# Kernel optimization log

Measured on AMD Instinct MI355X. Metric: run time of the kernel, lower is better.

## Reference

```python
import jax, jax.numpy as jnp
import numpy as np

B, N, H, HS, PH = 8, 384, 12, 768, 64
D = HS // H  # 64


def _ln(x, g, b, eps=1e-5):
    m = jnp.mean(x, axis=-1, keepdims=True)
    v = jnp.mean(jnp.square(x - m), axis=-1, keepdims=True)
    return (x - m) * jax.lax.rsqrt(v + eps) * g + b


def setup_inputs() -> dict:
    key = jax.random.key(0)
    ks = jax.random.split(key, 16)
    s = 0.02
    return {
        "nodes": jax.random.normal(ks[0], (B, N, HS), jnp.float32),
        "bias": jnp.zeros((B, 1, 1, N), jnp.float32),
        "paths": jax.random.normal(ks[1], (B, N, N, PH), jnp.float32),
        "Wq": jax.random.normal(ks[2], (HS, HS), jnp.float32) * s,
        "bq": jnp.zeros((HS,), jnp.float32),
        "Wk": jax.random.normal(ks[3], (HS, HS), jnp.float32) * s,
        "bk": jnp.zeros((HS,), jnp.float32),
        "Wv": jax.random.normal(ks[4], (HS, HS), jnp.float32) * s,
        "bv": jnp.zeros((HS,), jnp.float32),
        "Wsk": jax.random.normal(ks[5], (PH, D), jnp.float32) * s,
        "bsk": jnp.zeros((D,), jnp.float32),
        "Wsv": jax.random.normal(ks[6], (PH, D), jnp.float32) * s,
        "bsv": jnp.zeros((D,), jnp.float32),
        "Wo": jax.random.normal(ks[7], (HS, HS), jnp.float32) * s,
        "bo": jnp.zeros((HS,), jnp.float32),
        "ln_g": jnp.ones((HS,), jnp.float32),
        "ln_b": jnp.zeros((HS,), jnp.float32),
        "pln_g": jnp.ones((PH,), jnp.float32),
        "pln_b": jnp.zeros((PH,), jnp.float32),
    }


def reference(nodes, bias, paths, Wq, bq, Wk, bk, Wv, bv, Wsk, bsk, Wsv, bsv,
              Wo, bo, ln_g, ln_b, pln_g, pln_b):
    # q/k/v projections, split heads -> (B, H, N, D)
    def split(x):
        return x.reshape(B, N, H, D).transpose(0, 2, 1, 3)

    q = split(nodes @ Wq + bq)
    k = split(nodes @ Wk + bk)
    v = split(nodes @ Wv + bv)

    p = _ln(paths, pln_g, pln_b)            # (B, N, N, PH)
    struct_k = p @ Wsk + bsk                # (B, N, N, D)
    struct_v = p @ Wsv + bsv                # (B, N, N, D)

    q = q * (D ** -0.5)
    w = jnp.einsum('bhid,bhjd->bhij', q, k)           # content scores
    w = w + jnp.einsum('bhid,bijd->bhij', q, struct_k)  # structural scores
    w = jax.nn.softmax(w + bias, axis=-1)             # (B, H, N, N)

    out = jnp.einsum('bhij,bhjd->bhid', w, v) \
        + jnp.einsum('bhij,bijd->bhid', w, struct_v)  # (B, H, N, D)
    out = out.transpose(0, 2, 1, 3).reshape(B, N, HS)
    out = jax.nn.relu(out @ Wo + bo)
    # dropout p=0.0 -> identity
    return _ln(nodes + out, ln_g, ln_b), w
```

## Files before the change

kernel.cpp:

```cpp
#include <hip/hip_runtime.h>
#include <hip/hip_bf16.h>

typedef __hip_bfloat16 bf16;
typedef __attribute__((ext_vector_type(8))) short short8b;
typedef __attribute__((ext_vector_type(4))) float f32x4;

#define BB  8
#define NN  384
#define HH  12
#define HSZ 768
#define DD  64
#define PHH 64
#define PSTR 386
#define SWS  194

__device__ __forceinline__ float bflo(unsigned u){ union{unsigned q; float f;} c; c.q = u << 16;        return c.f; }
__device__ __forceinline__ float bfhi(unsigned u){ union{unsigned q; float f;} c; c.q = u & 0xffff0000u; return c.f; }

__device__ __forceinline__ unsigned pk2bf(float lo, float hi){
    union{float f; unsigned u;} a, b; a.f = lo; b.f = hi;
    unsigned ua = a.u + 0x7fffu + ((a.u >> 16) & 1u);
    unsigned ub = b.u + 0x7fffu + ((b.u >> 16) & 1u);
    return (ua >> 16) | (ub & 0xffff0000u);
}

union U8 { uint4 u; short8b v; };

__device__ __forceinline__ void pk32(const float4* p, uint4* o){
    #pragma unroll
    for (int e = 0; e < 4; e++) {
        float4 x = p[2*e], y = p[2*e+1];
        o[e].x = pk2bf(x.x, x.y); o[e].y = pk2bf(x.z, x.w);
        o[e].z = pk2bf(y.x, y.y); o[e].w = pk2bf(y.z, y.w);
    }
}

__global__ __launch_bounds__(256) void k_qkv(
    const float* __restrict__ nodes,
    const float* __restrict__ Wq, const float* __restrict__ bq,
    const float* __restrict__ Wk, const float* __restrict__ bk,
    const float* __restrict__ Wv, const float* __restrict__ bv,
    float* __restrict__ oq, float* __restrict__ okk, float* __restrict__ ov)
{
    const int which = blockIdx.z;
    const float* __restrict__ W   = which==0 ? Wq : (which==1 ? Wk : Wv);
    const float* __restrict__ bia = which==0 ? bq : (which==1 ? bk : bv);
    float* __restrict__ out       = which==0 ? oq : (which==1 ? okk : ov);
    const float scale = which==0 ? 0.125f : 1.0f;

    __shared__ __align__(16) unsigned Alds[128*20];
    __shared__ __align__(16) unsigned Blds[128*20];

    const int row0 = blockIdx.x * 128;
    const int col0 = blockIdx.y * 128;
    const int tid  = threadIdx.x;
    const int wv   = tid >> 6, lane = tid & 63;
    const int wm   = wv & 1,  wn   = wv >> 1;
    const int fr   = lane & 15, kg = lane >> 4;

    f32x4 acc[4][4];
    #pragma unroll
    for (int i=0;i<4;i++){
        #pragma unroll
        for (int j=0;j<4;j++){ acc[i][j][0]=0.f; acc[i][j][1]=0.f; acc[i][j][2]=0.f; acc[i][j][3]=0.f; }
    }

    for (int k0 = 0; k0 < HSZ; k0 += 32) {
        {
            const int m = tid >> 1, kh = tid & 1;
            const float4* ap = reinterpret_cast<const float4*>(nodes + (size_t)(row0 + m)*HSZ + k0 + kh*16);
            float4 a0 = ap[0], a1 = ap[1], a2 = ap[2], a3 = ap[3];
            uint4 p0, p1;
            p0.x = pk2bf(a0.x,a0.y); p0.y = pk2bf(a0.z,a0.w);
            p0.z = pk2bf(a1.x,a1.y); p0.w = pk2bf(a1.z,a1.w);
            p1.x = pk2bf(a2.x,a2.y); p1.y = pk2bf(a2.z,a2.w);
            p1.z = pk2bf(a3.x,a3.y); p1.w = pk2bf(a3.z,a3.w);
            *reinterpret_cast<uint4*>(&Alds[m*20 + kh*8    ]) = p0;
            *reinterpret_cast<uint4*>(&Alds[m*20 + kh*8 + 4]) = p1;
        }
        {
            const int n = tid & 127, kq = tid >> 7;
            const float* wp = W + (size_t)(k0 + kq*16)*HSZ + col0 + n;
            float x[16];
            #pragma unroll
            for (int j = 0; j < 16; j++) x[j] = wp[(size_t)j*HSZ];
            uint4 p0, p1;
            p0.x = pk2bf(x[0],x[1]);   p0.y = pk2bf(x[2],x[3]);
            p0.z = pk2bf(x[4],x[5]);   p0.w = pk2bf(x[6],x[7]);
            p1.x = pk2bf(x[8],x[9]);   p1.y = pk2bf(x[10],x[11]);
            p1.z = pk2bf(x[12],x[13]); p1.w = pk2bf(x[14],x[15]);
            *reinterpret_cast<uint4*>(&Blds[n*20 + kq*8    ]) = p0;
            *reinterpret_cast<uint4*>(&Blds[n*20 + kq*8 + 4]) = p1;
        }
        __syncthreads();
        U8 au[4], bu[4];
        #pragma unroll
        for (int t = 0; t < 4; t++) {
            au[t].u = *reinterpret_cast<const uint4*>(&Alds[(wm*64 + t*16 + fr)*20 + kg*4]);
            bu[t].u = *reinterpret_cast<const uint4*>(&Blds[(wn*64 + t*16 + fr)*20 + kg*4]);
        }
        #pragma unroll
        for (int mt = 0; mt < 4; mt++)
            #pragma unroll
            for (int nt = 0; nt < 4; nt++)
                acc[mt][nt] = __builtin_amdgcn_mfma_f32_16x16x32_bf16(
                    au[mt].v, bu[nt].v, acc[mt][nt], 0, 0, 0);
        __syncthreads();
    }
    #pragma unroll
    for (int nt = 0; nt < 4; nt++) {
        const int col = col0 + wn*64 + nt*16 + fr;
        const int h = col >> 6, d = col & 63;
        const float bv_ = bia[col];
        #pragma unroll
        for (int mt = 0; mt < 4; mt++) {
            #pragma unroll
            for (int r = 0; r < 4; r++) {
                const int m = row0 + wm*64 + mt*16 + kg*4 + r;
                const int b_ = m / NN, n_ = m % NN;
                out[(((size_t)b_*HH + h)*NN + n_)*DD + d] = (acc[mt][nt][r] + bv_) * scale;
            }
        }
    }
}

__global__ __launch_bounds__(256) void k_qsk(
    const float* __restrict__ q_s, const float* __restrict__ Wsk,
    float* __restrict__ qsk)
{
    __shared__ __align__(16) unsigned Alds[128*36];
    __shared__ __align__(16) unsigned Blds[64*36];
    const int row0 = blockIdx.x * 128;
    const int tid = threadIdx.x;
    const int wv = tid >> 6, lane = tid & 63;
    const int fr = lane & 15, kg = lane >> 4;

    {
        const int m = tid >> 1, kh = tid & 1;
        const float4* ap = reinterpret_cast<const float4*>(q_s + (size_t)(row0 + m)*DD + kh*32);
        uint4 pa[4]; pk32(ap, pa);
        #pragma unroll
        for (int e = 0; e < 4; e++)
            *reinterpret_cast<uint4*>(&Alds[m*36 + kh*16 + 4*e]) = pa[e];
    }
    {
        const int n = tid & 63, kq = tid >> 6;
        const float4* bp = reinterpret_cast<const float4*>(Wsk + (size_t)n*DD + kq*16);
        float4 b0 = bp[0], b1 = bp[1], b2 = bp[2], b3 = bp[3];
        uint4 p0, p1;
        p0.x = pk2bf(b0.x,b0.y); p0.y = pk2bf(b0.z,b0.w);
        p0.z = pk2bf(b1.x,b1.y); p0.w = pk2bf(b1.z,b1.w);
        p1.x = pk2bf(b2.x,b2.y); p1.y = pk2bf(b2.z,b2.w);
        p1.z = pk2bf(b3.x,b3.y); p1.w = pk2bf(b3.z,b3.w);
        *reinterpret_cast<uint4*>(&Blds[n*36 + kq*8    ]) = p0;
        *reinterpret_cast<uint4*>(&Blds[n*36 + kq*8 + 4]) = p1;
    }
    __syncthreads();

    f32x4 acc[2][4];
    #pragma unroll
    for (int i=0;i<2;i++){
        #pragma unroll
        for (int j=0;j<4;j++){ acc[i][j][0]=0.f; acc[i][j][1]=0.f; acc[i][j][2]=0.f; acc[i][j][3]=0.f; }
    }
    #pragma unroll
    for (int ks = 0; ks < 2; ks++) {
        U8 au[2], bu[4];
        #pragma unroll
        for (int mt = 0; mt < 2; mt++)
            au[mt].u = *reinterpret_cast<const uint4*>(&Alds[(wv*32 + mt*16 + fr)*36 + ks*16 + kg*4]);
        #pragma unroll
        for (int nt = 0; nt < 4; nt++)
            bu[nt].u = *reinterpret_cast<const uint4*>(&Blds[(nt*16 + fr)*36 + ks*16 + kg*4]);
        #pragma unroll
        for (int mt = 0; mt < 2; mt++)
            #pragma unroll
            for (int nt = 0; nt < 4; nt++)
                acc[mt][nt] = __builtin_amdgcn_mfma_f32_16x16x32_bf16(
                    au[mt].v, bu[nt].v, acc[mt][nt], 0, 0, 0);
    }
    #pragma unroll
    for (int nt = 0; nt < 4; nt++) {
        #pragma unroll
        for (int mt = 0; mt < 2; mt++) {
            #pragma unroll
            for (int r = 0; r < 4; r++) {
                const int m = row0 + wv*32 + mt*16 + kg*4 + r;
                qsk[(size_t)m*DD + nt*16 + fr] = acc[mt][nt][r];
            }
        }
    }
}

__global__ __launch_bounds__(256) void k_scores(
    const float* __restrict__ q_s, const float* __restrict__ kk_, float* __restrict__ wc)
{
    const int bh = blockIdx.z;
    __shared__ __align__(16) unsigned Alds[128*36];
    __shared__ __align__(16) unsigned Blds[128*36];
    const int i0 = blockIdx.x * 128, j0 = blockIdx.y * 128;
    const int tid = threadIdx.x;
    const int wv  = tid >> 6, lane = tid & 63;
    const int wm  = wv & 1,  wn   = wv >> 1;
    const int fr  = lane & 15, kg = lane >> 4;

    {
        const int m = tid >> 1, kh = tid & 1;
        const float4* ap = reinterpret_cast<const float4*>(q_s + ((size_t)bh*NN + i0 + m)*DD + kh*32);
        const float4* bp = reinterpret_cast<const float4*>(kk_ + ((size_t)bh*NN + j0 + m)*DD + kh*32);
        uint4 pa[4], pbq[4];
        pk32(ap, pa);
        pk32(bp, pbq);
        #pragma unroll
        for (int e = 0; e < 4; e++) {
            *reinterpret_cast<uint4*>(&Alds[m*36 + kh*16 + 4*e]) = pa[e];
            *reinterpret_cast<uint4*>(&Blds[m*36 + kh*16 + 4*e]) = pbq[e];
        }
    }
    __syncthreads();

    f32x4 acc[4][4];
    #pragma unroll
    for (int i=0;i<4;i++){
        #pragma unroll
        for (int j=0;j<4;j++){ acc[i][j][0]=0.f; acc[i][j][1]=0.f; acc[i][j][2]=0.f; acc[i][j][3]=0.f; }
    }
    #pragma unroll
    for (int ks = 0; ks < 2; ks++) {
        U8 au[4], bu[4];
        #pragma unroll
        for (int t = 0; t < 4; t++) {
            au[t].u = *reinterpret_cast<const uint4*>(&Alds[(wm*64 + t*16 + fr)*36 + ks*16 + kg*4]);
            bu[t].u = *reinterpret_cast<const uint4*>(&Blds[(wn*64 + t*16 + fr)*36 + ks*16 + kg*4]);
        }
        #pragma unroll
        for (int mt = 0; mt < 4; mt++)
            #pragma unroll
            for (int nt = 0; nt < 4; nt++)
                acc[mt][nt] = __builtin_amdgcn_mfma_f32_16x16x32_bf16(
                    au[mt].v, bu[nt].v, acc[mt][nt], 0, 0, 0);
    }
    #pragma unroll
    for (int nt = 0; nt < 4; nt++) {
        const int j = j0 + wn*64 + nt*16 + fr;
        #pragma unroll
        for (int mt = 0; mt < 4; mt++) {
            #pragma unroll
            for (int r = 0; r < 4; r++) {
                const int i = i0 + wm*64 + mt*16 + kg*4 + r;
                wc[((size_t)bh*NN + i)*NN + j] = acc[mt][nt][r];
            }
        }
    }
}

__global__ __launch_bounds__(384) void k_soft(
    const float* __restrict__ paths, const float* __restrict__ bias,
    const float* __restrict__ pg, const float* __restrict__ pb,
    const float* __restrict__ wc, const float* __restrict__ qsk,
    float* __restrict__ pagg, float* __restrict__ w_out)
{
    const int bi = blockIdx.x;
    const int b = bi / NN, i = bi % NN;
    __shared__ __align__(16) unsigned pLNT[32 * PSTR];
    __shared__ __align__(16) unsigned sw32[16 * SWS];
    __shared__ __align__(16) unsigned qskA[16 * 36];
    __shared__ float redM[6][16];
    __shared__ float redS[6][16];
    __shared__ float pgf[64], pbf[64];
    const int tid  = threadIdx.x;
    const int wv   = tid >> 6, lane = tid & 63;
    const int g    = lane >> 4, c = lane & 15;
    const int jbase = wv*64 + c;

    float x[64];
    {
        const float4* src = reinterpret_cast<const float4*>(paths + ((size_t)bi * NN + tid) * PHH);
        #pragma unroll
        for (int t = 0; t < 16; t++) {
            float4 u = src[t];
            x[4*t]=u.x; x[4*t+1]=u.y; x[4*t+2]=u.z; x[4*t+3]=u.w;
        }
    }
    float wcv[4][4], biasj[4];
    #pragma unroll
    for (int nt = 0; nt < 4; nt++) {
        const int j = jbase + nt*16;
        biasj[nt] = bias[b*NN + j];
        #pragma unroll
        for (int r = 0; r < 4; r++) {
            const int h = g*4 + r;
            wcv[nt][r] = (h < HH) ? wc[((size_t)(b*HH + h)*NN + i)*NN + j] : 0.f;
        }
    }
    if (tid < 64) { pgf[tid] = pg[tid]; pbf[tid] = pb[tid]; }
    {
        const int h = tid >> 5, t2 = tid & 31;
        const size_t r0 = ((size_t)(b*HH + h)*NN + i)*DD;
        const float q0 = qsk[r0 + 2*t2], q1 = qsk[r0 + 2*t2 + 1];
        qskA[h*36 + t2] = pk2bf(q0, q1);
        if (tid < 144) qskA[432 + tid] = 0u;
    }
    __syncthreads();

    {
        float m0 = 0.f, m1 = 0.f;
        #pragma unroll
        for (int t = 0; t < 32; t++){ m0 += x[2*t]; m1 += x[2*t+1]; }
        const float m = (m0+m1)*(1.f/64.f);
        float v0 = 0.f, v1 = 0.f;
        #pragma unroll
        for (int t = 0; t < 32; t++){
            float a = x[2*t]-m, d = x[2*t+1]-m;
            v0 = fmaf(a,a,v0); v1 = fmaf(d,d,v1);
        }
        const float rs = rsqrtf((v0+v1)*(1.f/64.f) + 1e-5f);
        #pragma unroll
        for (int w = 0; w < 32; w++){
            const float lo = (x[2*w  ]-m)*rs*pgf[2*w  ] + pbf[2*w  ];
            const float hi = (x[2*w+1]-m)*rs*pgf[2*w+1] + pbf[2*w+1];
            pLNT[w*PSTR + tid] = pk2bf(lo, hi);
        }
    }
    __syncthreads();

    f32x4 sc[4];
    #pragma unroll
    for (int nt=0;nt<4;nt++){ sc[nt][0]=0.f; sc[nt][1]=0.f; sc[nt][2]=0.f; sc[nt][3]=0.f; }
    #pragma unroll
    for (int kh = 0; kh < 2; kh++) {
        U8 a; a.u = *reinterpret_cast<const uint4*>(&qskA[c*36 + kh*16 + g*4]);
        #pragma unroll
        for (int nt = 0; nt < 4; nt++) {
            const unsigned* pb_ = &pLNT[(kh*16 + g*4)*PSTR + jbase + nt*16];
            uint4 bw;
            bw.x = pb_[0]; bw.y = pb_[PSTR]; bw.z = pb_[2*PSTR]; bw.w = pb_[3*PSTR];
            U8 bb; bb.u = bw;
            sc[nt] = __builtin_amdgcn_mfma_f32_16x16x32_bf16(a.v, bb.v, sc[nt], 0, 0, 0);
        }
    }
    #pragma unroll
    for (int nt = 0; nt < 4; nt++)
        #pragma unroll
        for (int r = 0; r < 4; r++)
            sc[nt][r] += wcv[nt][r] + biasj[nt];

    float e_[4][4], inv_[4];
    {
        float mr[4];
        #pragma unroll
        for (int r = 0; r < 4; r++) {
            float m2 = fmaxf(fmaxf(sc[0][r], sc[1][r]), fmaxf(sc[2][r], sc[3][r]));
            #pragma unroll
            for (int o = 1; o <= 8; o <<= 1) m2 = fmaxf(m2, __shfl_xor(m2, o, 64));
            mr[r] = m2;
        }
        if (c == 0) {
            #pragma unroll
            for (int r = 0; r < 4; r++) redM[wv][g*4 + r] = mr[r];
        }
        __syncthreads();
        #pragma unroll
        for (int r = 0; r < 4; r++) {
            float Mv = redM[0][g*4 + r];
            #pragma unroll
            for (int w2 = 1; w2 < 6; w2++) Mv = fmaxf(Mv, redM[w2][g*4 + r]);
            float s2 = 0.f;
            #pragma unroll
            for (int nt = 0; nt < 4; nt++){ e_[nt][r] = __expf(sc[nt][r] - Mv); s2 += e_[nt][r]; }
            #pragma unroll
            for (int o = 1; o <= 8; o <<= 1) s2 += __shfl_xor(s2, o, 64);
            mr[r] = s2;
        }
        if (c == 0) {
            #pragma unroll
            for (int r = 0; r < 4; r++) redS[wv][g*4 + r] = mr[r];
        }
        __syncthreads();
        #pragma unroll
        for (int r = 0; r < 4; r++) {
            float Sv = redS[0][g*4 + r];
            #pragma unroll
            for (int w2 = 1; w2 < 6; w2++) Sv += redS[w2][g*4 + r];
            inv_[r] = 1.f / Sv;
        }
    }
    #pragma unroll
    for (int nt = 0; nt < 4; nt++) {
        const int j = jbase + nt*16;
        #pragma unroll
        for (int r = 0; r < 4; r++) {
            const int h = g*4 + r;
            const float wgt = e_[nt][r] * inv_[r];
            if (h < HH) w_out[((size_t)(b*HH + h)*NN + i)*NN + j] = wgt;
            const float oth = __shfl_xor(wgt, 1, 64);
            if ((c & 1) == 0) sw32[h*SWS + (j >> 1)] = pk2bf(wgt, oth);
        }
    }
    __syncthreads();

    if (wv < 4) {
        f32x4 pa; pa[0]=0.f; pa[1]=0.f; pa[2]=0.f; pa[3]=0.f;
        const int prow = 8*wv + (c >> 1);
        const bool hi = (c & 1);
        #pragma unroll 4
        for (int kt = 0; kt < 12; kt++) {
            uint2 a0 = *reinterpret_cast<const uint2*>(&sw32[c*SWS + kt*16 + g*4]);
            uint2 a1 = *reinterpret_cast<const uint2*>(&sw32[c*SWS + kt*16 + g*4 + 2]);
            U8 af; af.u.x = a0.x; af.u.y = a0.y; af.u.z = a1.x; af.u.w = a1.y;
            const unsigned* pr = &pLNT[prow*PSTR + 32*kt + 8*g];
            uint2 w01 = *reinterpret_cast<const uint2*>(&pr[0]);
            uint2 w23 = *reinterpret_cast<const uint2*>(&pr[2]);
            uint2 w45 = *reinterpret_cast<const uint2*>(&pr[4]);
            uint2 w67 = *reinterpret_cast<const uint2*>(&pr[6]);
            uint4 bw;
            if (hi) {
                bw.x = (w01.x >> 16) | (w01.y & 0xffff0000u);
                bw.y = (w23.x >> 16) | (w23.y & 0xffff0000u);
                bw.z = (w45.x >> 16) | (w45.y & 0xffff0000u);
                bw.w = (w67.x >> 16) | (w67.y & 0xffff0000u);
            } else {
                bw.x = (w01.x & 0xffffu) | (w01.y << 16);
                bw.y = (w23.x & 0xffffu) | (w23.y << 16);
                bw.z = (w45.x & 0xffffu) | (w45.y << 16);
                bw.w = (w67.x & 0xffffu) | (w67.y << 16);
            }
            U8 bf_; bf_.u = bw;
            pa = __builtin_amdgcn_mfma_f32_16x16x32_bf16(af.v, bf_.v, pa, 0, 0, 0);
        }
        #pragma unroll
        for (int r = 0; r < 4; r++) {
            const int h = g*4 + r;
            if (h < HH)
                pagg[((size_t)(b*HH + h)*NN + i)*DD + 16*wv + c] = pa[r];
        }
    }
}

__global__ __launch_bounds__(256) void k_av(
    const float* __restrict__ w, const float* __restrict__ v_,
    const float* __restrict__ pagg, const float* __restrict__ Wsv,
    const float* __restrict__ bsv, float* __restrict__ attn)
{
    const int bh = blockIdx.y;
    const int b = bh / HH, h = bh % HH;
    const int i0 = blockIdx.x * 128;
    __shared__ __align__(16) unsigned Alds[128*36];
    __shared__ __align__(16) unsigned Blds[64*36];
    const int tid = threadIdx.x;
    const int wv  = tid >> 6, lane = tid & 63;
    const int fr  = lane & 15, kg = lane >> 4;

    f32x4 acc[2][4];
    #pragma unroll
    for (int i=0;i<2;i++){
        #pragma unroll
        for (int j=0;j<4;j++){ acc[i][j][0]=0.f; acc[i][j][1]=0.f; acc[i][j][2]=0.f; acc[i][j][3]=0.f; }
    }

    for (int step = 0; step < 7; step++) {
        const int j0 = step * 64;
        {
            const int m = tid >> 1, kh = tid & 1;
            const float4* ap = (step < 6)
                ? reinterpret_cast<const float4*>(w    + ((size_t)bh*NN + i0 + m)*NN  + j0 + kh*32)
                : reinterpret_cast<const float4*>(pagg + ((size_t)bh*NN + i0 + m)*PHH + kh*32);
            uint4 pa[4];
            pk32(ap, pa);
            #pragma unroll
            for (int e = 0; e < 4; e++)
                *reinterpret_cast<uint4*>(&Alds[m*36 + kh*16 + 4*e]) = pa[e];
        }
        {
            const int d = tid & 63, kq = tid >> 6;
            const float* vp = (step < 6)
                ? (v_  + ((size_t)bh*NN + j0 + kq*16)*DD + d)
                : (Wsv + (size_t)(kq*16)*DD + d);
            float x[16];
            #pragma unroll
            for (int t = 0; t < 16; t++) x[t] = vp[(size_t)t*DD];
            uint4 p0,p1;
            p0.x=pk2bf(x[0],x[1]);   p0.y=pk2bf(x[2],x[3]);
            p0.z=pk2bf(x[4],x[5]);   p0.w=pk2bf(x[6],x[7]);
            p1.x=pk2bf(x[8],x[9]);   p1.y=pk2bf(x[10],x[11]);
            p1.z=pk2bf(x[12],x[13]); p1.w=pk2bf(x[14],x[15]);
            *reinterpret_cast<uint4*>(&Blds[d*36 + kq*8    ]) = p0;
            *reinterpret_cast<uint4*>(&Blds[d*36 + kq*8 + 4]) = p1;
        }
        __syncthreads();
        #pragma unroll
        for (int ks = 0; ks < 2; ks++) {
            U8 au[2], bu[4];
            #pragma unroll
            for (int mt = 0; mt < 2; mt++)
                au[mt].u = *reinterpret_cast<const uint4*>(&Alds[(wv*32 + mt*16 + fr)*36 + ks*16 + kg*4]);
            #pragma unroll
            for (int nt = 0; nt < 4; nt++)
                bu[nt].u = *reinterpret_cast<const uint4*>(&Blds[(nt*16 + fr)*36 + ks*16 + kg*4]);
            #pragma unroll
            for (int mt = 0; mt < 2; mt++)
                #pragma unroll
                for (int nt = 0; nt < 4; nt++)
                    acc[mt][nt] = __builtin_amdgcn_mfma_f32_16x16x32_bf16(
                        au[mt].v, bu[nt].v, acc[mt][nt], 0, 0, 0);
        }
        __syncthreads();
    }
    #pragma unroll
    for (int nt = 0; nt < 4; nt++) {
        const int d = nt*16 + fr;
        const float bv_ = bsv[d];
        #pragma unroll
        for (int mt = 0; mt < 2; mt++) {
            #pragma unroll
            for (int r = 0; r < 4; r++) {
                const int i = i0 + wv*32 + mt*16 + kg*4 + r;
                attn[((size_t)b*NN + i)*HSZ + h*DD + d] = acc[mt][nt][r] + bv_;
            }
        }
    }
}

__global__ __launch_bounds__(256) void k_proj(
    const float* __restrict__ attn, const float* __restrict__ Wo,
    const float* __restrict__ bo, const float* __restrict__ nodes,
    float* __restrict__ tres)
{
    __shared__ __align__(16) unsigned Alds[128*20];
    __shared__ __align__(16) unsigned Blds[128*20];

    const int row0 = blockIdx.x * 128;
    const int col0 = blockIdx.y * 128;
    const int tid  = threadIdx.x;
    const int wv   = tid >> 6, lane = tid & 63;
    const int wm   = wv & 1,  wn   = wv >> 1;
    const int fr   = lane & 15, kg = lane >> 4;

    f32x4 acc[4][4];
    #pragma unroll
    for (int i=0;i<4;i++){
        #pragma unroll
        for (int j=0;j<4;j++){ acc[i][j][0]=0.f; acc[i][j][1]=0.f; acc[i][j][2]=0.f; acc[i][j][3]=0.f; }
    }

    for (int k0 = 0; k0 < HSZ; k0 += 32) {
        {
            const int m = tid >> 1, kh = tid & 1;
            const float4* ap = reinterpret_cast<const float4*>(attn + (size_t)(row0 + m)*HSZ + k0 + kh*16);
            float4 a0 = ap[0], a1 = ap[1], a2 = ap[2], a3 = ap[3];
            uint4 p0, p1;
            p0.x = pk2bf(a0.x,a0.y); p0.y = pk2bf(a0.z,a0.w);
            p0.z = pk2bf(a1.x,a1.y); p0.w = pk2bf(a1.z,a1.w);
            p1.x = pk2bf(a2.x,a2.y); p1.y = pk2bf(a2.z,a2.w);
            p1.z = pk2bf(a3.x,a3.y); p1.w = pk2bf(a3.z,a3.w);
            *reinterpret_cast<uint4*>(&Alds[m*20 + kh*8    ]) = p0;
            *reinterpret_cast<uint4*>(&Alds[m*20 + kh*8 + 4]) = p1;
        }
        {
            const int n = tid & 127, kq = tid >> 7;
            const float* wp = Wo + (size_t)(k0 + kq*16)*HSZ + col0 + n;
            float x[16];
            #pragma unroll
            for (int j = 0; j < 16; j++) x[j] = wp[(size_t)j*HSZ];
            uint4 p0, p1;
            p0.x = pk2bf(x[0],x[1]);   p0.y = pk2bf(x[2],x[3]);
            p0.z = pk2bf(x[4],x[5]);   p0.w = pk2bf(x[6],x[7]);
            p1.x = pk2bf(x[8],x[9]);   p1.y = pk2bf(x[10],x[11]);
            p1.z = pk2bf(x[12],x[13]); p1.w = pk2bf(x[14],x[15]);
            *reinterpret_cast<uint4*>(&Blds[n*20 + kq*8    ]) = p0;
            *reinterpret_cast<uint4*>(&Blds[n*20 + kq*8 + 4]) = p1;
        }
        __syncthreads();
        U8 au[4], bu[4];
        #pragma unroll
        for (int t = 0; t < 4; t++) {
            au[t].u = *reinterpret_cast<const uint4*>(&Alds[(wm*64 + t*16 + fr)*20 + kg*4]);
            bu[t].u = *reinterpret_cast<const uint4*>(&Blds[(wn*64 + t*16 + fr)*20 + kg*4]);
        }
        #pragma unroll
        for (int mt = 0; mt < 4; mt++)
            #pragma unroll
            for (int nt = 0; nt < 4; nt++)
                acc[mt][nt] = __builtin_amdgcn_mfma_f32_16x16x32_bf16(
                    au[mt].v, bu[nt].v, acc[mt][nt], 0, 0, 0);
        __syncthreads();
    }
    #pragma unroll
    for (int nt = 0; nt < 4; nt++) {
        const int col = col0 + wn*64 + nt*16 + fr;
        const float bov = bo[col];
        #pragma unroll
        for (int mt = 0; mt < 4; mt++) {
            #pragma unroll
            for (int r = 0; r < 4; r++) {
                const int m = row0 + wm*64 + mt*16 + kg*4 + r;
                const float val = fmaxf(acc[mt][nt][r] + bov, 0.f) + nodes[(size_t)m*HSZ + col];
                tres[(size_t)m*HSZ + col] = val;
            }
        }
    }
}

__global__ __launch_bounds__(256) void k_ln(
    const float* __restrict__ tres, const float* __restrict__ g,
    const float* __restrict__ bta, float* __restrict__ out0)
{
    const int row  = blockIdx.x * 4 + (threadIdx.x >> 6);
    const int lane = threadIdx.x & 63;
    const float4* x4 = reinterpret_cast<const float4*>(tres + (size_t)row * HSZ);
    float4 v[3];
    #pragma unroll
    for (int t = 0; t < 3; t++) v[t] = x4[lane + t*64];
    float s = 0.f;
    #pragma unroll
    for (int t = 0; t < 3; t++) s += v[t].x + v[t].y + v[t].z + v[t].w;
    #pragma unroll
    for (int o = 32; o > 0; o >>= 1) s += __shfl_xor(s, o, 64);
    const float m = s * (1.f/768.f);
    float vs = 0.f;
    #pragma unroll
    for (int t = 0; t < 3; t++) {
        float a = v[t].x-m, b = v[t].y-m, c = v[t].z-m, d = v[t].w-m;
        vs += a*a + b*b + c*c + d*d;
    }
    #pragma unroll
    for (int o = 32; o > 0; o >>= 1) vs += __shfl_xor(vs, o, 64);
    const float rs = rsqrtf(vs * (1.f/768.f) + 1e-5f);
    const float4* g4 = reinterpret_cast<const float4*>(g);
    const float4* b4 = reinterpret_cast<const float4*>(bta);
    float4* o4 = reinterpret_cast<float4*>(out0 + (size_t)row * HSZ);
    #pragma unroll
    for (int t = 0; t < 3; t++) {
        const int idx = lane + t*64;
        float4 gg = g4[idx], bb = b4[idx], o;
        o.x = (v[t].x-m)*rs*gg.x + bb.x;
        o.y = (v[t].y-m)*rs*gg.y + bb.y;
        o.z = (v[t].z-m)*rs*gg.z + bb.z;
        o.w = (v[t].w-m)*rs*gg.w + bb.w;
        o4[idx] = o;
    }
}

extern "C" void kernel_launch(void* const* d_in, const int* in_sizes, int n_in,
                              void* d_out, int out_size, void* d_ws, size_t ws_size,
                              hipStream_t stream)
{
    (void)in_sizes; (void)n_in; (void)out_size; (void)ws_size;
    const float* nodes = (const float*)d_in[0];
    const float* bias  = (const float*)d_in[1];
    const float* paths = (const float*)d_in[2];
    const float* Wq = (const float*)d_in[3];
    const float* bq = (const float*)d_in[4];
    const float* Wk = (const float*)d_in[5];
    const float* bk = (const float*)d_in[6];
    const float* Wv = (const float*)d_in[7];
    const float* bv = (const float*)d_in[8];
    const float* Wsk= (const float*)d_in[9];
    const float* Wsv= (const float*)d_in[11];
    const float* bsv= (const float*)d_in[12];
    const float* Wo = (const float*)d_in[13];
    const float* bo = (const float*)d_in[14];
    const float* lng= (const float*)d_in[15];
    const float* lnb= (const float*)d_in[16];
    const float* plg= (const float*)d_in[17];
    const float* plb= (const float*)d_in[18];

    float* ws   = (float*)d_ws;
    float* q_s  = ws;
    float* kbuf = ws + 2359296;
    float* vbuf = ws + 4718592;
    float* qsk  = ws + 7077888;
    float* wc   = ws + 9474048;
    float* attn = q_s;
    float* pagg = kbuf;
    float* tres = wc;

    float* out0 = (float*)d_out;
    float* wout = out0 + (size_t)BB*NN*HSZ;

    hipLaunchKernelGGL(k_qkv,    dim3(24,6,3), dim3(256), 0, stream,
                       nodes, Wq,bq, Wk,bk, Wv,bv, q_s, kbuf, vbuf);
    hipLaunchKernelGGL(k_qsk,    dim3(288),    dim3(256), 0, stream,
                       q_s, Wsk, qsk);
    hipLaunchKernelGGL(k_scores, dim3(3,3,96), dim3(256), 0, stream,
                       q_s, kbuf, wc);
    hipLaunchKernelGGL(k_soft,   dim3(3072),   dim3(384), 0, stream,
                       paths, bias, plg, plb, wc, qsk, pagg, wout);
    hipLaunchKernelGGL(k_av,     dim3(3,96),   dim3(256), 0, stream,
                       wout, vbuf, pagg, Wsv, bsv, attn);
    hipLaunchKernelGGL(k_proj,   dim3(24,6),   dim3(256), 0, stream,
                       attn, Wo, bo, nodes, tres);
    hipLaunchKernelGGL(k_ln,     dim3(768),    dim3(256), 0, stream,
                       tres, lng, lnb, out0);
}
```

Baseline: 283.6 us.

## Double k_soft block size, splitting each path row LayerNorm across two threads

```diff
diff --git a/kernel.cpp b/kernel.cpp
--- a/kernel.cpp
+++ b/kernel.cpp
@@ -254,7 +254,7 @@
     }
 }
 
-__global__ __launch_bounds__(384) void k_soft(
+__global__ __launch_bounds__(768) void k_soft(
     const float* __restrict__ paths, const float* __restrict__ bias,
     const float* __restrict__ pg, const float* __restrict__ pb,
     const float* __restrict__ wc, const float* __restrict__ qsk,
@@ -265,26 +265,28 @@
     __shared__ __align__(16) unsigned pLNT[32 * PSTR];
     __shared__ __align__(16) unsigned sw32[16 * SWS];
     __shared__ __align__(16) unsigned qskA[16 * 36];
-    __shared__ float redM[6][16];
-    __shared__ float redS[6][16];
+    __shared__ float redM[12][16];
+    __shared__ float redS[12][16];
     __shared__ float pgf[64], pbf[64];
     const int tid  = threadIdx.x;
     const int wv   = tid >> 6, lane = tid & 63;
     const int g    = lane >> 4, c = lane & 15;
-    const int jbase = wv*64 + c;
-
-    float x[64];
+    const int jbase = wv*32 + c;
+
+    const int jrow = tid >> 1, hf = tid & 1;
+    float x[32];
     {
-        const float4* src = reinterpret_cast<const float4*>(paths + ((size_t)bi * NN + tid) * PHH);
-        #pragma unroll
-        for (int t = 0; t < 16; t++) {
+        const float4* src = reinterpret_cast<const float4*>(
+            paths + ((size_t)bi * NN + jrow) * PHH + hf*32);
+        #pragma unroll
+        for (int t = 0; t < 8; t++) {
             float4 u = src[t];
             x[4*t]=u.x; x[4*t+1]=u.y; x[4*t+2]=u.z; x[4*t+3]=u.w;
         }
     }
-    float wcv[4][4], biasj[4];
-    #pragma unroll
-    for (int nt = 0; nt < 4; nt++) {
+    float wcv[2][4], biasj[2];
+    #pragma unroll
+    for (int nt = 0; nt < 2; nt++) {
         const int j = jbase + nt*16;
         biasj[nt] = bias[b*NN + j];
         #pragma unroll
@@ -294,7 +296,7 @@
         }
     }
     if (tid < 64) { pgf[tid] = pg[tid]; pbf[tid] = pb[tid]; }
-    {
+    if (tid < 384) {
         const int h = tid >> 5, t2 = tid & 31;
         const size_t r0 = ((size_t)(b*HH + h)*NN + i)*DD;
         const float q0 = qsk[r0 + 2*t2], q1 = qsk[r0 + 2*t2 + 1];
@@ -304,34 +306,35 @@
     __syncthreads();
 
     {
-        float m0 = 0.f, m1 = 0.f;
-        #pragma unroll
-        for (int t = 0; t < 32; t++){ m0 += x[2*t]; m1 += x[2*t+1]; }
-        const float m = (m0+m1)*(1.f/64.f);
-        float v0 = 0.f, v1 = 0.f;
-        #pragma unroll
-        for (int t = 0; t < 32; t++){
-            float a = x[2*t]-m, d = x[2*t+1]-m;
-            v0 = fmaf(a,a,v0); v1 = fmaf(d,d,v1);
-        }
-        const float rs = rsqrtf((v0+v1)*(1.f/64.f) + 1e-5f);
-        #pragma unroll
-        for (int w = 0; w < 32; w++){
-            const float lo = (x[2*w  ]-m)*rs*pgf[2*w  ] + pbf[2*w  ];
-            const float hi = (x[2*w+1]-m)*rs*pgf[2*w+1] + pbf[2*w+1];
-            pLNT[w*PSTR + tid] = pk2bf(lo, hi);
+        float m0 = 0.f;
+        #pragma unroll
+        for (int t = 0; t < 32; t++) m0 += x[t];
+        const float mo = __shfl_xor(m0, 1, 64);
+        const float m = (m0 + mo) * (1.f/64.f);
+        float v0 = 0.f;
+        #pragma unroll
+        for (int t = 0; t < 32; t++){ float d = x[t]-m; v0 = fmaf(d,d,v0); }
+        const float vo = __shfl_xor(v0, 1, 64);
+        const float rs = rsqrtf((v0+vo)*(1.f/64.f) + 1e-5f);
+        #pragma unroll
+        for (int t = 0; t < 16; t++){
+            const int w = hf*16 + t;
+            const int ph = hf*32 + 2*t;
+            const float lo = (x[2*t  ]-m)*rs*pgf[ph  ] + pbf[ph  ];
+            const float hi = (x[2*t+1]-m)*rs*pgf[ph+1] + pbf[ph+1];
+            pLNT[w*PSTR + jrow] = pk2bf(lo, hi);
         }
     }
     __syncthreads();
 
-    f32x4 sc[4];
-    #pragma unroll
-    for (int nt=0;nt<4;nt++){ sc[nt][0]=0.f; sc[nt][1]=0.f; sc[nt][2]=0.f; sc[nt][3]=0.f; }
+    f32x4 sc[2];
+    #pragma unroll
+    for (int nt=0;nt<2;nt++){ sc[nt][0]=0.f; sc[nt][1]=0.f; sc[nt][2]=0.f; sc[nt][3]=0.f; }
     #pragma unroll
     for (int kh = 0; kh < 2; kh++) {
         U8 a; a.u = *reinterpret_cast<const uint4*>(&qskA[c*36 + kh*16 + g*4]);
         #pragma unroll
-        for (int nt = 0; nt < 4; nt++) {
+        for (int nt = 0; nt < 2; nt++) {
             const unsigned* pb_ = &pLNT[(kh*16 + g*4)*PSTR + jbase + nt*16];
             uint4 bw;
             bw.x = pb_[0]; bw.y = pb_[PSTR]; bw.z = pb_[2*PSTR]; bw.w = pb_[3*PSTR];
@@ -340,17 +343,17 @@
         }
     }
     #pragma unroll
-    for (int nt = 0; nt < 4; nt++)
+    for (int nt = 0; nt < 2; nt++)
         #pragma unroll
         for (int r = 0; r < 4; r++)
             sc[nt][r] += wcv[nt][r] + biasj[nt];
 
-    float e_[4][4], inv_[4];
+    float e_[2][4], inv_[4];
     {
         float mr[4];
         #pragma unroll
         for (int r = 0; r < 4; r++) {
-            float m2 = fmaxf(fmaxf(sc[0][r], sc[1][r]), fmaxf(sc[2][r], sc[3][r]));
+            float m2 = fmaxf(sc[0][r], sc[1][r]);
             #pragma unroll
             for (int o = 1; o <= 8; o <<= 1) m2 = fmaxf(m2, __shfl_xor(m2, o, 64));
             mr[r] = m2;
@@ -364,10 +367,10 @@
         for (int r = 0; r < 4; r++) {
             float Mv = redM[0][g*4 + r];
             #pragma unroll
-            for (int w2 = 1; w2 < 6; w2++) Mv = fmaxf(Mv, redM[w2][g*4 + r]);
+            for (int w2 = 1; w2 < 12; w2++) Mv = fmaxf(Mv, redM[w2][g*4 + r]);
             float s2 = 0.f;
             #pragma unroll
-            for (int nt = 0; nt < 4; nt++){ e_[nt][r] = __expf(sc[nt][r] - Mv); s2 += e_[nt][r]; }
+            for (int nt = 0; nt < 2; nt++){ e_[nt][r] = __expf(sc[nt][r] - Mv); s2 += e_[nt][r]; }
             #pragma unroll
             for (int o = 1; o <= 8; o <<= 1) s2 += __shfl_xor(s2, o, 64);
             mr[r] = s2;
@@ -381,12 +384,12 @@
         for (int r = 0; r < 4; r++) {
             float Sv = redS[0][g*4 + r];
             #pragma unroll
-            for (int w2 = 1; w2 < 6; w2++) Sv += redS[w2][g*4 + r];
+            for (int w2 = 1; w2 < 12; w2++) Sv += redS[w2][g*4 + r];
             inv_[r] = 1.f / Sv;
         }
     }
     #pragma unroll
-    for (int nt = 0; nt < 4; nt++) {
+    for (int nt = 0; nt < 2; nt++) {
         const int j = jbase + nt*16;
         #pragma unroll
         for (int r = 0; r < 4; r++) {
@@ -684,7 +687,7 @@
                        q_s, Wsk, qsk);
     hipLaunchKernelGGL(k_scores, dim3(3,3,96), dim3(256), 0, stream,
                        q_s, kbuf, wc);
-    hipLaunchKernelGGL(k_soft,   dim3(3072),   dim3(384), 0, stream,
+    hipLaunchKernelGGL(k_soft,   dim3(3072),   dim3(768), 0, stream,
                        paths, bias, plg, plb, wc, qsk, pagg, wout);
     hipLaunchKernelGGL(k_av,     dim3(3,96),   dim3(256), 0, stream,
                        wout, vbuf, pagg, Wsv, bsv, attn);
```

Result: no change. 280.1 us, median of 2 (-1.2%).

## Process two query rows per k_soft block, prefetching the second paths row

Applied to the files above, without the earlier changes.

```diff
diff --git a/kernel.cpp b/kernel.cpp
--- a/kernel.cpp
+++ b/kernel.cpp
@@ -260,8 +260,9 @@
     const float* __restrict__ wc, const float* __restrict__ qsk,
     float* __restrict__ pagg, float* __restrict__ w_out)
 {
-    const int bi = blockIdx.x;
-    const int b = bi / NN, i = bi % NN;
+    const int blk = blockIdx.x;
+    const int b   = blk / 192;
+    const int i0  = (blk % 192) * 2;
     __shared__ __align__(16) unsigned pLNT[32 * PSTR];
     __shared__ __align__(16) unsigned sw32[16 * SWS];
     __shared__ __align__(16) unsigned qskA[16 * 36];
@@ -273,16 +274,17 @@
     const int g    = lane >> 4, c = lane & 15;
     const int jbase = wv*64 + c;
 
-    float x[64];
+    float x0[64];
     {
-        const float4* src = reinterpret_cast<const float4*>(paths + ((size_t)bi * NN + tid) * PHH);
+        const float4* src = reinterpret_cast<const float4*>(
+            paths + ((size_t)(b*NN + i0) * NN + tid) * PHH);
         #pragma unroll
         for (int t = 0; t < 16; t++) {
             float4 u = src[t];
-            x[4*t]=u.x; x[4*t+1]=u.y; x[4*t+2]=u.z; x[4*t+3]=u.w;
-        }
-    }
-    float wcv[4][4], biasj[4];
+            x0[4*t]=u.x; x0[4*t+1]=u.y; x0[4*t+2]=u.z; x0[4*t+3]=u.w;
+        }
+    }
+    float biasj[4], wcv0[4][4], wcv1[4][4];
     #pragma unroll
     for (int nt = 0; nt < 4; nt++) {
         const int j = jbase + nt*16;
@@ -290,149 +292,303 @@
         #pragma unroll
         for (int r = 0; r < 4; r++) {
             const int h = g*4 + r;
-            wcv[nt][r] = (h < HH) ? wc[((size_t)(b*HH + h)*NN + i)*NN + j] : 0.f;
-        }
-    }
+            const size_t ro = ((size_t)(b*HH + h)*NN + i0)*NN + j;
+            wcv0[nt][r] = (h < HH) ? wc[ro]      : 0.f;
+            wcv1[nt][r] = (h < HH) ? wc[ro + NN] : 0.f;
+        }
+    }
+    const int hA = tid >> 5, t2 = tid & 31;
+    const size_t rA0 = ((size_t)(b*HH + hA)*NN + i0)*DD;
+    const float qa0 = qsk[rA0 + 2*t2],      qa1 = qsk[rA0 + 2*t2 + 1];
+    const float qb0 = qsk[rA0 + DD + 2*t2], qb1 = qsk[rA0 + DD + 2*t2 + 1];
+
     if (tid < 64) { pgf[tid] = pg[tid]; pbf[tid] = pb[tid]; }
-    {
-        const int h = tid >> 5, t2 = tid & 31;
-        const size_t r0 = ((size_t)(b*HH + h)*NN + i)*DD;
-        const float q0 = qsk[r0 + 2*t2], q1 = qsk[r0 + 2*t2 + 1];
-        qskA[h*36 + t2] = pk2bf(q0, q1);
-        if (tid < 144) qskA[432 + tid] = 0u;
-    }
+    qskA[hA*36 + t2] = pk2bf(qa0, qa1);
+    if (tid < 144) qskA[432 + tid] = 0u;
     __syncthreads();
 
     {
         float m0 = 0.f, m1 = 0.f;
         #pragma unroll
-        for (int t = 0; t < 32; t++){ m0 += x[2*t]; m1 += x[2*t+1]; }
+        for (int t = 0; t < 32; t++){ m0 += x0[2*t]; m1 += x0[2*t+1]; }
         const float m = (m0+m1)*(1.f/64.f);
         float v0 = 0.f, v1 = 0.f;
         #pragma unroll
         for (int t = 0; t < 32; t++){
-            float a = x[2*t]-m, d = x[2*t+1]-m;
+            float a = x0[2*t]-m, d = x0[2*t+1]-m;
             v0 = fmaf(a,a,v0); v1 = fmaf(d,d,v1);
         }
         const float rs = rsqrtf((v0+v1)*(1.f/64.f) + 1e-5f);
         #pragma unroll
         for (int w = 0; w < 32; w++){
-            const float lo = (x[2*w  ]-m)*rs*pgf[2*w  ] + pbf[2*w  ];
-            const float hi = (x[2*w+1]-m)*rs*pgf[2*w+1] + pbf[2*w+1];
+            const float lo = (x0[2*w  ]-m)*rs*pgf[2*w  ] + pbf[2*w  ];
+            const float hi = (x0[2*w+1]-m)*rs*pgf[2*w+1] + pbf[2*w+1];
             pLNT[w*PSTR + tid] = pk2bf(lo, hi);
         }
     }
+    float x1[64];
+    {
+        const float4* src = reinterpret_cast<const float4*>(
+            paths + ((size_t)(b*NN + i0 + 1) * NN + tid) * PHH);
+        #pragma unroll
+        for (int t = 0; t < 16; t++) {
+            float4 u = src[t];
+            x1[4*t]=u.x; x1[4*t+1]=u.y; x1[4*t+2]=u.z; x1[4*t+3]=u.w;
+        }
+        #pragma unroll
+        for (int t = 0; t < 64; t++) asm volatile("" : "+v"(x1[t]));
+    }
     __syncthreads();
 
-    f32x4 sc[4];
-    #pragma unroll
-    for (int nt=0;nt<4;nt++){ sc[nt][0]=0.f; sc[nt][1]=0.f; sc[nt][2]=0.f; sc[nt][3]=0.f; }
-    #pragma unroll
-    for (int kh = 0; kh < 2; kh++) {
-        U8 a; a.u = *reinterpret_cast<const uint4*>(&qskA[c*36 + kh*16 + g*4]);
+    {
+        f32x4 sc[4];
+        #pragma unroll
+        for (int nt=0;nt<4;nt++){ sc[nt][0]=0.f; sc[nt][1]=0.f; sc[nt][2]=0.f; sc[nt][3]=0.f; }
+        #pragma unroll
+        for (int kh = 0; kh < 2; kh++) {
+            U8 a; a.u = *reinterpret_cast<const uint4*>(&qskA[c*36 + kh*16 + g*4]);
+            #pragma unroll
+            for (int nt = 0; nt < 4; nt++) {
+                const unsigned* pb_ = &pLNT[(kh*16 + g*4)*PSTR + jbase + nt*16];
+                uint4 bw;
+                bw.x = pb_[0]; bw.y = pb_[PSTR]; bw.z = pb_[2*PSTR]; bw.w = pb_[3*PSTR];
+                U8 bb; bb.u = bw;
+                sc[nt] = __builtin_amdgcn_mfma_f32_16x16x32_bf16(a.v, bb.v, sc[nt], 0, 0, 0);
+            }
+        }
+        #pragma unroll
+        for (int nt = 0; nt < 4; nt++)
+            #pragma unroll
+            for (int r = 0; r < 4; r++)
+                sc[nt][r] += wcv0[nt][r] + biasj[nt];
+
+        float e_[4][4], inv_[4];
+        {
+            float mr[4];
+            #pragma unroll
+            for (int r = 0; r < 4; r++) {
+                float m2 = fmaxf(fmaxf(sc[0][r], sc[1][r]), fmaxf(sc[2][r], sc[3][r]));
+                #pragma unroll
+                for (int o = 1; o <= 8; o <<= 1) m2 = fmaxf(m2, __shfl_xor(m2, o, 64));
+                mr[r] = m2;
+            }
+            if (c == 0) {
+                #pragma unroll
+                for (int r = 0; r < 4; r++) redM[wv][g*4 + r] = mr[r];
+            }
+            __syncthreads();
+            #pragma unroll
+            for (int r = 0; r < 4; r++) {
+                float Mv = redM[0][g*4 + r];
+                #pragma unroll
+                for (int w2 = 1; w2 < 6; w2++) Mv = fmaxf(Mv, redM[w2][g*4 + r]);
+                float s2 = 0.f;
+                #pragma unroll
+                for (int nt = 0; nt < 4; nt++){ e_[nt][r] = __expf(sc[nt][r] - Mv); s2 += e_[nt][r]; }
+                #pragma unroll
+                for (int o = 1; o <= 8; o <<= 1) s2 += __shfl_xor(s2, o, 64);
+                mr[r] = s2;
+            }
+            if (c == 0) {
+                #pragma unroll
+                for (int r = 0; r < 4; r++) redS[wv][g*4 + r] = mr[r];
+            }
+            __syncthreads();
+            #pragma unroll
+            for (int r = 0; r < 4; r++) {
+                float Sv = redS[0][g*4 + r];
+                #pragma unroll
+                for (int w2 = 1; w2 < 6; w2++) Sv += redS[w2][g*4 + r];
+                inv_[r] = 1.f / Sv;
+            }
+        }
         #pragma unroll
         for (int nt = 0; nt < 4; nt++) {
-            const unsigned* pb_ = &pLNT[(kh*16 + g*4)*PSTR + jbase + nt*16];
-            uint4 bw;
-            bw.x = pb_[0]; bw.y = pb_[PSTR]; bw.z = pb_[2*PSTR]; bw.w = pb_[3*PSTR];
-            U8 bb; bb.u = bw;
-            sc[nt] = __builtin_amdgcn_mfma_f32_16x16x32_bf16(a.v, bb.v, sc[nt], 0, 0, 0);
-        }
-    }
-    #pragma unroll
-    for (int nt = 0; nt < 4; nt++)
-        #pragma unroll
-        for (int r = 0; r < 4; r++)
-            sc[nt][r] += wcv[nt][r] + biasj[nt];
-
-    float e_[4][4], inv_[4];
+            const int j = jbase + nt*16;
+            #pragma unroll
+            for (int r = 0; r < 4; r++) {
+                const int h = g*4 + r;
+                const float wgt = e_[nt][r] * inv_[r];
+                if (h < HH) w_out[((size_t)(b*HH + h)*NN + i0)*NN + j] = wgt;
+                const float oth = __shfl_xor(wgt, 1, 64);
+                if ((c & 1) == 0) sw32[h*SWS + (j >> 1)] = pk2bf(wgt, oth);
+            }
+        }
+        __syncthreads();
+
+        qskA[hA*36 + t2] = pk2bf(qb0, qb1);
+        if (wv < 4) {
+            f32x4 pa; pa[0]=0.f; pa[1]=0.f; pa[2]=0.f; pa[3]=0.f;
+            const int prow = 8*wv + (c >> 1);
+            const bool hi = (c & 1);
+            #pragma unroll 4
+            for (int kt = 0; kt < 12; kt++) {
+                uint2 a0 = *reinterpret_cast<const uint2*>(&sw32[c*SWS + kt*16 + g*4]);
+                uint2 a1 = *reinterpret_cast<const uint2*>(&sw32[c*SWS + kt*16 + g*4 + 2]);
+                U8 af; af.u.x = a0.x; af.u.y = a0.y; af.u.z = a1.x; af.u.w = a1.y;
+                const unsigned* pr = &pLNT[prow*PSTR + 32*kt + 8*g];
+                uint2 w01 = *reinterpret_cast<const uint2*>(&pr[0]);
+                uint2 w23 = *reinterpret_cast<const uint2*>(&pr[2]);
+                uint2 w45 = *reinterpret_cast<const uint2*>(&pr[4]);
+                uint2 w67 = *reinterpret_cast<const uint2*>(&pr[6]);
+                uint4 bw;
+                if (hi) {
+                    bw.x = (w01.x >> 16) | (w01.y & 0xffff0000u);
+                    bw.y = (w23.x >> 16) | (w23.y & 0xffff0000u);
+                    bw.z = (w45.x >> 16) | (w45.y & 0xffff0000u);
+                    bw.w = (w67.x >> 16) | (w67.y & 0xffff0000u);
+                } else {
+                    bw.x = (w01.x & 0xffffu) | (w01.y << 16);
+                    bw.y = (w23.x & 0xffffu) | (w23.y << 16);
+                    bw.z = (w45.x & 0xffffu) | (w45.y << 16);
+                    bw.w = (w67.x & 0xffffu) | (w67.y << 16);
+                }
+                U8 bf_; bf_.u = bw;
+                pa = __builtin_amdgcn_mfma_f32_16x16x32_bf16(af.v, bf_.v, pa, 0, 0, 0);
+            }
+            #pragma unroll
+            for (int r = 0; r < 4; r++) {
+                const int h = g*4 + r;
+                if (h < HH)
+                    pagg[((size_t)(b*HH + h)*NN + i0)*DD + 16*wv + c] = pa[r];
+            }
+        }
+    }
+    __syncthreads();
+
     {
-        float mr[4];
-        #pragma unroll
-        for (int r = 0; r < 4; r++) {
-            float m2 = fmaxf(fmaxf(sc[0][r], sc[1][r]), fmaxf(sc[2][r], sc[3][r]));
-            #pragma unroll
-            for (int o = 1; o <= 8; o <<= 1) m2 = fmaxf(m2, __shfl_xor(m2, o, 64));
-            mr[r] = m2;
-        }
-        if (c == 0) {
-            #pragma unroll
-            for (int r = 0; r < 4; r++) redM[wv][g*4 + r] = mr[r];
+        float m0 = 0.f, m1 = 0.f;
+        #pragma unroll
+        for (int t = 0; t < 32; t++){ m0 += x1[2*t]; m1 += x1[2*t+1]; }
+        const float m = (m0+m1)*(1.f/64.f);
+        float v0 = 0.f, v1 = 0.f;
+        #pragma unroll
+        for (int t = 0; t < 32; t++){
+            float a = x1[2*t]-m, d = x1[2*t+1]-m;
+            v0 = fmaf(a,a,v0); v1 = fmaf(d,d,v1);
+        }
+        const float rs = rsqrtf((v0+v1)*(1.f/64.f) + 1e-5f);
+        #pragma unroll
+        for (int w = 0; w < 32; w++){
+            const float lo = (x1[2*w  ]-m)*rs*pgf[2*w  ] + pbf[2*w  ];
+            const float hi = (x1[2*w+1]-m)*rs*pgf[2*w+1] + pbf[2*w+1];
+            pLNT[w*PSTR + tid] = pk2bf(lo, hi);
+        }
+    }
+    __syncthreads();
+
+    {
+        const int i1 = i0 + 1;
+        f32x4 sc[4];
+        #pragma unroll
+        for (int nt=0;nt<4;nt++){ sc[nt][0]=0.f; sc[nt][1]=0.f; sc[nt][2]=0.f; sc[nt][3]=0.f; }
+        #pragma unroll
+        for (int kh = 0; kh < 2; kh++) {
+            U8 a; a.u = *reinterpret_cast<const uint4*>(&qskA[c*36 + kh*16 + g*4]);
+            #pragma unroll
+            for (int nt = 0; nt < 4; nt++) {
+                const unsigned* pb_ = &pLNT[(kh*16 + g*4)*PSTR + jbase + nt*16];
+                uint4 bw;
+                bw.x = pb_[0]; bw.y = pb_[PSTR]; bw.z = pb_[2*PSTR]; bw.w = pb_[3*PSTR];
+                U8 bb; bb.u = bw;
+                sc[nt] = __builtin_amdgcn_mfma_f32_16x16x32_bf16(a.v, bb.v, sc[nt], 0, 0, 0);
+            }
+        }
+        #pragma unroll
+        for (int nt = 0; nt < 4; nt++)
+            #pragma unroll
+            for (int r = 0; r < 4; r++)
+                sc[nt][r] += wcv1[nt][r] + biasj[nt];
+
+        float e_[4][4], inv_[4];
+        {
+            float mr[4];
+            #pragma unroll
+            for (int r = 0; r < 4; r++) {
+                float m2 = fmaxf(fmaxf(sc[0][r], sc[1][r]), fmaxf(sc[2][r], sc[3][r]));
+                #pragma unroll
+                for (int o = 1; o <= 8; o <<= 1) m2 = fmaxf(m2, __shfl_xor(m2, o, 64));
+                mr[r] = m2;
+            }
+            if (c == 0) {
+                #pragma unroll
+                for (int r = 0; r < 4; r++) redM[wv][g*4 + r] = mr[r];
+            }
+            __syncthreads();
+            #pragma unroll
+            for (int r = 0; r < 4; r++) {
+                float Mv = redM[0][g*4 + r];
+                #pragma unroll
+                for (int w2 = 1; w2 < 6; w2++) Mv = fmaxf(Mv, redM[w2][g*4 + r]);
+                float s2 = 0.f;
+                #pragma unroll
+                for (int nt = 0; nt < 4; nt++){ e_[nt][r] = __expf(sc[nt][r] - Mv); s2 += e_[nt][r]; }
+                #pragma unroll
+                for (int o = 1; o <= 8; o <<= 1) s2 += __shfl_xor(s2, o, 64);
+                mr[r] = s2;
+            }
+            if (c == 0) {
+                #pragma unroll
+                for (int r = 0; r < 4; r++) redS[wv][g*4 + r] = mr[r];
+            }
+            __syncthreads();
+            #pragma unroll
+            for (int r = 0; r < 4; r++) {
+                float Sv = redS[0][g*4 + r];
+                #pragma unroll
+                for (int w2 = 1; w2 < 6; w2++) Sv += redS[w2][g*4 + r];
+                inv_[r] = 1.f / Sv;
+            }
+        }
+        #pragma unroll
+        for (int nt = 0; nt < 4; nt++) {
+            const int j = jbase + nt*16;
+            #pragma unroll
+            for (int r = 0; r < 4; r++) {
+                const int h = g*4 + r;
+                const float wgt = e_[nt][r] * inv_[r];
+                if (h < HH) w_out[((size_t)(b*HH + h)*NN + i1)*NN + j] = wgt;
+                const float oth = __shfl_xor(wgt, 1, 64);
+                if ((c & 1) == 0) sw32[h*SWS + (j >> 1)] = pk2bf(wgt, oth);
+            }
         }
         __syncthreads();
-        #pragma unroll
-        for (int r = 0; r < 4; r++) {
-            float Mv = redM[0][g*4 + r];
-            #pragma unroll
-            for (int w2 = 1; w2 < 6; w2++) Mv = fmaxf(Mv, redM[w2][g*4 + r]);
-            float s2 = 0.f;
-            #pragma unroll
-            for (int nt = 0; nt < 4; nt++){ e_[nt][r] = __expf(sc[nt][r] - Mv); s2 += e_[nt][r]; }
-            #pragma unroll
-            for (int o = 1; o <= 8; o <<= 1) s2 += __shfl_xor(s2, o, 64);
-            mr[r] = s2;
-        }
-        if (c == 0) {
-            #pragma unroll
-            for (int r = 0; r < 4; r++) redS[wv][g*4 + r] = mr[r];
-        }
-        __syncthreads();
-        #pragma unroll
-        for (int r = 0; r < 4; r++) {
-            float Sv = redS[0][g*4 + r];
-            #pragma unroll
-            for (int w2 = 1; w2 < 6; w2++) Sv += redS[w2][g*4 + r];
-            inv_[r] = 1.f / Sv;
-        }
-    }
-    #pragma unroll
-    for (int nt = 0; nt < 4; nt++) {
-        const int j = jbase + nt*16;
-        #pragma unroll
-        for (int r = 0; r < 4; r++) {
-            const int h = g*4 + r;
-            const float wgt = e_[nt][r] * inv_[r];
-            if (h < HH) w_out[((size_t)(b*HH + h)*NN + i)*NN + j] = wgt;
-            const float oth = __shfl_xor(wgt, 1, 64);
-            if ((c & 1) == 0) sw32[h*SWS + (j >> 1)] = pk2bf(wgt, oth);
-        }
-    }
-    __syncthreads();
-
-    if (wv < 4) {
-        f32x4 pa; pa[0]=0.f; pa[1]=0.f; pa[2]=0.f; pa[3]=0.f;
-        const int prow = 8*wv + (c >> 1);
-        const bool hi = (c & 1);
-        #pragma unroll 4
-        for (int kt = 0; kt < 12; kt++) {
-            uint2 a0 = *reinterpret_cast<const uint2*>(&sw32[c*SWS + kt*16 + g*4]);
-            uint2 a1 = *reinterpret_cast<const uint2*>(&sw32[c*SWS + kt*16 + g*4 + 2]);
-            U8 af; af.u.x = a0.x; af.u.y = a0.y; af.u.z = a1.x; af.u.w = a1.y;
-            const unsigned* pr = &pLNT[prow*PSTR + 32*kt + 8*g];
-            uint2 w01 = *reinterpret_cast<const uint2*>(&pr[0]);
-            uint2 w23 = *reinterpret_cast<const uint2*>(&pr[2]);
-            uint2 w45 = *reinterpret_cast<const uint2*>(&pr[4]);
-            uint2 w67 = *reinterpret_cast<const uint2*>(&pr[6]);
-            uint4 bw;
-            if (hi) {
-                bw.x = (w01.x >> 16) | (w01.y & 0xffff0000u);
-                bw.y = (w23.x >> 16) | (w23.y & 0xffff0000u);
-                bw.z = (w45.x >> 16) | (w45.y & 0xffff0000u);
-                bw.w = (w67.x >> 16) | (w67.y & 0xffff0000u);
-            } else {
-                bw.x = (w01.x & 0xffffu) | (w01.y << 16);
-                bw.y = (w23.x & 0xffffu) | (w23.y << 16);
-                bw.z = (w45.x & 0xffffu) | (w45.y << 16);
-                bw.w = (w67.x & 0xffffu) | (w67.y << 16);
-            }
-            U8 bf_; bf_.u = bw;
-            pa = __builtin_amdgcn_mfma_f32_16x16x32_bf16(af.v, bf_.v, pa, 0, 0, 0);
-        }
-        #pragma unroll
-        for (int r = 0; r < 4; r++) {
-            const int h = g*4 + r;
-            if (h < HH)
-                pagg[((size_t)(b*HH + h)*NN + i)*DD + 16*wv + c] = pa[r];
+
+        if (wv < 4) {
+            f32x4 pa; pa[0]=0.f; pa[1]=0.f; pa[2]=0.f; pa[3]=0.f;
+            const int prow = 8*wv + (c >> 1);
+            const bool hi = (c & 1);
+            #pragma unroll 4
+            for (int kt = 0; kt < 12; kt++) {
+                uint2 a0 = *reinterpret_cast<const uint2*>(&sw32[c*SWS + kt*16 + g*4]);
+                uint2 a1 = *reinterpret_cast<const uint2*>(&sw32[c*SWS + kt*16 + g*4 + 2]);
+                U8 af; af.u.x = a0.x; af.u.y = a0.y; af.u.z = a1.x; af.u.w = a1.y;
+                const unsigned* pr = &pLNT[prow*PSTR + 32*kt + 8*g];
+                uint2 w01 = *reinterpret_cast<const uint2*>(&pr[0]);
+                uint2 w23 = *reinterpret_cast<const uint2*>(&pr[2]);
+                uint2 w45 = *reinterpret_cast<const uint2*>(&pr[4]);
+                uint2 w67 = *reinterpret_cast<const uint2*>(&pr[6]);
+                uint4 bw;
+                if (hi) {
+                    bw.x = (w01.x >> 16) | (w01.y & 0xffff0000u);
+                    bw.y = (w23.x >> 16) | (w23.y & 0xffff0000u);
+                    bw.z = (w45.x >> 16) | (w45.y & 0xffff0000u);
+                    bw.w = (w67.x >> 16) | (w67.y & 0xffff0000u);
+                } else {
+                    bw.x = (w01.x & 0xffffu) | (w01.y << 16);
+                    bw.y = (w23.x & 0xffffu) | (w23.y << 16);
+                    bw.z = (w45.x & 0xffffu) | (w45.y << 16);
+                    bw.w = (w67.x & 0xffffu) | (w67.y << 16);
+                }
+                U8 bf_; bf_.u = bw;
+                pa = __builtin_amdgcn_mfma_f32_16x16x32_bf16(af.v, bf_.v, pa, 0, 0, 0);
+            }
+            #pragma unroll
+            for (int r = 0; r < 4; r++) {
+                const int h = g*4 + r;
+                if (h < HH)
+                    pagg[((size_t)(b*HH + h)*NN + i1)*DD + 16*wv + c] = pa[r];
+            }
         }
     }
 }
@@ -684,7 +840,7 @@
                        q_s, Wsk, qsk);
     hipLaunchKernelGGL(k_scores, dim3(3,3,96), dim3(256), 0, stream,
                        q_s, kbuf, wc);
-    hipLaunchKernelGGL(k_soft,   dim3(3072),   dim3(384), 0, stream,
+    hipLaunchKernelGGL(k_soft,   dim3(1536),   dim3(384), 0, stream,
                        paths, bias, plg, plb, wc, qsk, pagg, wout);
     hipLaunchKernelGGL(k_av,     dim3(3,96),   dim3(256), 0, stream,
                        wout, vbuf, pagg, Wsv, bsv, attn);
```

Result: slower. 295.9 us (+4.3%).
